# Optimization experiments

Measured on AMD Instinct MI355X. Metric: run time of the kernel, lower is better.

Reference implementation:

```python
import jax, jax.numpy as jnp
import numpy as np

EPS_MEAN = 1e-10


def setup_inputs() -> dict:
    key = jax.random.key(0)
    ks = jax.random.split(key, 16)
    B, N, F, D = 2, 512, 128, 3
    s = lambda fan_in: 1.0 / np.sqrt(fan_in)
    return {
        "h": jax.random.normal(ks[0], (B, N, F), jnp.float32),
        "coord": jax.random.normal(ks[1], (B, N, D), jnp.float32),
        "mask": jnp.ones((B, N), jnp.float32),
        "edge_w1": jax.random.normal(ks[2], (2 * F + 1, F), jnp.float32) * s(2 * F + 1),
        "edge_b1": jnp.zeros((F,), jnp.float32),
        "edge_w2": jax.random.normal(ks[3], (F, F), jnp.float32) * s(F),
        "edge_b2": jnp.zeros((F,), jnp.float32),
        "node_w1": jax.random.normal(ks[4], (2 * F, F), jnp.float32) * s(2 * F),
        "node_b1": jnp.zeros((F,), jnp.float32),
        "node_w2": jax.random.normal(ks[5], (F, F), jnp.float32) * s(F),
        "node_b2": jnp.zeros((F,), jnp.float32),
        "coord_w1": jax.random.normal(ks[6], (F, F), jnp.float32) * s(F),
        "coord_b1": jnp.zeros((F,), jnp.float32),
        # xavier_uniform with gain=0.001 -> tiny weights
        "coord_w2": jax.random.normal(ks[7], (F, 1), jnp.float32) * 0.001 * s(F),
    }


def reference(h, coord, mask, edge_w1, edge_b1, edge_w2, edge_b2,
              node_w1, node_b1, node_w2, node_b2,
              coord_w1, coord_b1, coord_w2):
    silu = jax.nn.silu
    B, N, F = h.shape
    # mask inputs
    h = h * mask[:, :, None]
    coord = coord * mask[:, :, None]
    mask2d = mask[:, :, None] * mask[:, None, :]            # [B,N,N]

    # coord2radial
    coord_diff = coord[:, :, None] - coord[:, None]          # [B,N,N,3]
    radial = jnp.sum(coord_diff ** 2, axis=-1, keepdims=True)  # [B,N,N,1]
    radial = radial * mask2d[..., None]
    coord_diff = coord_diff * mask2d[..., None]

    # edge model: source[b,i,j]=h[b,j], target[b,i,j]=h[b,i]
    source = jnp.broadcast_to(h[:, None, :, :], (B, N, N, F))
    target = jnp.broadcast_to(h[:, :, None, :], (B, N, N, F))
    edge_in = jnp.concatenate([source, target, radial], axis=-1)  # [B,N,N,2F+1]
    m = silu(edge_in @ edge_w1 + edge_b1)
    m = silu(m @ edge_w2 + edge_b2)                          # [B,N,N,F]
    m = m * mask2d[..., None]

    # coord model
    embed = silu(m @ coord_w1 + coord_b1) @ coord_w2         # [B,N,N,1]
    trans = coord_diff * embed * mask2d[..., None]           # [B,N,N,3]
    denom = jnp.sum(mask2d, axis=2, keepdims=True) + EPS_MEAN  # [B,N,1]
    coord_new = coord + jnp.sum(trans, axis=2) / denom
    coord_new = coord_new * mask[:, :, None]

    # node model
    agg = jnp.sum(m, axis=2)                                 # [B,N,F]
    node_in = jnp.concatenate([h, agg], axis=-1) * mask[:, :, None]
    out = silu(node_in @ node_w1 + node_b1) @ node_w2 + node_b2
    h_new = (h + out) * mask[:, :, None]

    return h_new, coord_new
```

## Files before the change

kernel.cpp:

```cpp
#include <hip/hip_runtime.h>

#define B_ 2
#define N_ 512
#define F_ 128
#define MSTRIDE 136

typedef __attribute__((ext_vector_type(8))) short short8;
typedef __attribute__((ext_vector_type(4))) float floatx4;

__device__ __forceinline__ float fsilu(float x) {
    float e = __expf(-x);
    return x * __builtin_amdgcn_rcpf(1.0f + e);
}
__device__ __forceinline__ unsigned pack2(float a, float b) {
    return __builtin_amdgcn_perm(__float_as_uint(b) + 0x8000u,
                                 __float_as_uint(a) + 0x8000u, 0x07060302u);
}

__global__ __launch_bounds__(256) void egcl_prep(
        const float* __restrict__ h, const float* __restrict__ mask,
        const float* __restrict__ ew1, const float* __restrict__ ew2,
        const float* __restrict__ cw1,
        float* __restrict__ Hs, float* __restrict__ Ht,
        unsigned short* __restrict__ W2P, unsigned short* __restrict__ WcP,
        float* __restrict__ msum) {
    __shared__ float hm[4 * F_];
    const int blk = blockIdx.x, tid = threadIdx.x;
    if (blk < 256) {
        const int r0 = blk * 4;
        hm[tid]       = h[r0 * F_ + tid]       * mask[r0 + (tid >> 7)];
        hm[tid + 256] = h[r0 * F_ + 256 + tid] * mask[r0 + 2 + (tid >> 7)];
        __syncthreads();
        const int col = tid & 127, half = tid >> 7;
        const float* W = ew1 + half * F_ * F_ + col;
        float a0 = 0.f, a1 = 0.f, a2 = 0.f, a3 = 0.f;
#pragma unroll 8
        for (int k = 0; k < F_; ++k) {
            float w = W[k * F_];
            a0 += hm[k] * w;
            a1 += hm[F_ + k] * w;
            a2 += hm[2 * F_ + k] * w;
            a3 += hm[3 * F_ + k] * w;
        }
        float* dst = half ? Ht : Hs;
        dst[(r0 + 0) * F_ + col] = a0;
        dst[(r0 + 1) * F_ + col] = a1;
        dst[(r0 + 2) * F_ + col] = a2;
        dst[(r0 + 3) * F_ + col] = a3;
    } else if (blk < 272) {
        const int wsel = (blk - 256) >> 3;
        const int mt = (blk - 256) & 7;
        const float* src = wsel ? cw1 : ew2;
        unsigned short* dst = wsel ? WcP : W2P;
        const int ln = tid & 63, kk = tid >> 6;
        const int qq = ln >> 4, ll = ln & 15;
#pragma unroll
        for (int rep = 0; rep < 2; ++rep) {
            const int krow = kk * 32 + qq * 8 + rep * 4;
            float f0 = src[(krow + 0) * F_ + mt * 16 + ll];
            float f1 = src[(krow + 1) * F_ + mt * 16 + ll];
            float f2 = src[(krow + 2) * F_ + mt * 16 + ll];
            float f3 = src[(krow + 3) * F_ + mt * 16 + ll];
            uint2 u = make_uint2(pack2(f0, f1), pack2(f2, f3));
            *(uint2*)(dst + ((mt * 4 + kk) * 64 + ln) * 8 + rep * 4) = u;
        }
    } else {
        const int bb = blk - 272;
        float v = mask[bb * N_ + tid] + mask[bb * N_ + 256 + tid];
        v += __shfl_xor(v, 1);  v += __shfl_xor(v, 2);
        v += __shfl_xor(v, 4);  v += __shfl_xor(v, 8);
        v += __shfl_xor(v, 16); v += __shfl_xor(v, 32);
        const int wave = tid >> 6, lane = tid & 63;
        if (lane == 0) hm[wave] = v;
        __syncthreads();
        if (tid == 0) msum[bb] = hm[0] + hm[1] + hm[2] + hm[3];
    }
}

#define L_M1   0
#define L_M    34816
#define L_HB   69632
#define L_W1R  70144
#define L_EMBP 70656
#define L_AGG  72704
#define L_HIN  73728
#define L_AGGT 74240
#define L_TL   74752
#define L_NP   75264
#define L_CSW  76288
#define L_TOTAL 76320

__global__ __launch_bounds__(512, 2) void egcl_main(
        const float* __restrict__ h, const float* __restrict__ coord,
        const float* __restrict__ mask,
        const float* __restrict__ eb1, const float* __restrict__ eb2,
        const float* __restrict__ cb1, const float* __restrict__ cw2,
        const float* __restrict__ nw1, const float* __restrict__ nb1,
        const float* __restrict__ nw2, const float* __restrict__ nb2,
        const float* __restrict__ ew1,
        const float* __restrict__ Hs, const float* __restrict__ Ht,
        const unsigned short* __restrict__ W2P,
        const unsigned short* __restrict__ WcP,
        const float* __restrict__ msum,
        float* __restrict__ out_h, float* __restrict__ out_coord) {
    extern __shared__ char smem[];
    unsigned short* m1s = (unsigned short*)(smem + L_M1);
    unsigned short* ms  = (unsigned short*)(smem + L_M);
    float* HB    = (float*)(smem + L_HB);
    float* W1R   = (float*)(smem + L_W1R);
    float* embp  = (float*)(smem + L_EMBP);
    float* aggs2 = (float*)(smem + L_AGG);
    float* hin   = (float*)(smem + L_HIN);
    float* aggt  = (float*)(smem + L_AGGT);
    float* tl    = (float*)(smem + L_TL);
    float* np    = (float*)(smem + L_NP);
    float* csw   = (float*)(smem + L_CSW);

    const int tid  = threadIdx.x;
    const int bk   = blockIdx.x;
    const int wave = tid >> 6, lane = tid & 63;
    const int q = lane >> 4, l15 = lane & 15;
    const int wg = wave & 3;
    const int g  = wave >> 2;

    short8 w2f[2][4], wcf[2][4];
#pragma unroll
    for (int s = 0; s < 2; ++s)
#pragma unroll
        for (int kk = 0; kk < 4; ++kk) {
            w2f[s][kk] = *(const short8*)(W2P + (((2 * wg + s) * 4 + kk) * 64 + lane) * 8);
            wcf[s][kk] = *(const short8*)(WcP + (((2 * wg + s) * 4 + kk) * 64 + lane) * 8);
        }
    floatx4 e2b[2], c1b[2], w2c[2];
#pragma unroll
    for (int s = 0; s < 2; ++s) {
        e2b[s] = *(const floatx4*)(eb2 + wg * 32 + s * 16 + q * 4);
        c1b[s] = *(const floatx4*)(cb1 + wg * 32 + s * 16 + q * 4);
        w2c[s] = *(const floatx4*)(cw2 + wg * 32 + s * 16 + q * 4);
    }
    const int kseg = tid & 15, jq4 = tid >> 4;

    for (int ii = 0; ii < 2; ++ii) {
        const int bi = bk + ii * 512;
        const int b  = bi >> 9;
        const float mask_i = mask[bi];
        __syncthreads();
        if (tid < F_) {
            HB[tid]  = Ht[bi * F_ + tid] + eb1[tid];
            W1R[tid] = ew1[2 * F_ * F_ + tid];
            hin[tid] = h[bi * F_ + tid] * mask_i;
        }
        const float cmi0 = coord[bi * 3 + 0] * mask_i;
        const float cmi1 = coord[bi * 3 + 1] * mask_i;
        const float cmi2 = coord[bi * 3 + 2] * mask_i;
        __syncthreads();
        float hbk[8], w1k[8];
        {
            const floatx4* hp = (const floatx4*)(HB + kseg * 8);
            const floatx4* wp = (const floatx4*)(W1R + kseg * 8);
            floatx4 a = hp[0], bb2 = hp[1], cc = wp[0], dd = wp[1];
#pragma unroll
            for (int t = 0; t < 4; ++t) {
                hbk[t] = a[t]; hbk[4 + t] = bb2[t];
                w1k[t] = cc[t]; w1k[4 + t] = dd[t];
            }
        }
        floatx4 agg0 = {0.f, 0.f, 0.f, 0.f}, agg1 = {0.f, 0.f, 0.f, 0.f};
        float cs0 = 0.f, cs1 = 0.f, cs2 = 0.f;

        for (int p = 0; p < 4; ++p) {
#pragma unroll
            for (int r = 0; r < 4; ++r) {
                int row = jq4 * 4 + r;
                int jg = b * N_ + p * 128 + row;
                float mj = mask[jg];
                float c0 = coord[jg * 3 + 0] * mj;
                float c1 = coord[jg * 3 + 1] * mj;
                float c2 = coord[jg * 3 + 2] * mj;
                float d0 = cmi0 - c0, d1 = cmi1 - c1, d2 = cmi2 - c2;
                float f2 = mask_i * mj;
                float rad = (d0 * d0 + d1 * d1 + d2 * d2) * f2;
                const floatx4* hsp = (const floatx4*)(Hs + jg * F_ + kseg * 8);
                floatx4 h0 = hsp[0], h1 = hsp[1];
                float x[8];
#pragma unroll
                for (int t = 0; t < 4; ++t) {
                    x[t]     = fsilu(h0[t] + hbk[t]     + rad * w1k[t]);
                    x[4 + t] = fsilu(h1[t] + hbk[4 + t] + rad * w1k[4 + t]);
                }
                union { short8 s8; unsigned u[4]; } pu;
                pu.u[0] = pack2(x[0], x[1]); pu.u[1] = pack2(x[2], x[3]);
                pu.u[2] = pack2(x[4], x[5]); pu.u[3] = pack2(x[6], x[7]);
                *(short8*)(m1s + row * MSTRIDE + kseg * 8) = pu.s8;
            }
            __syncthreads();
#pragma unroll
            for (int jt = 0; jt < 4; ++jt) {
                const int jrow = g * 64 + jt * 16 + l15;
                const unsigned short* m1r = m1s + jrow * MSTRIDE;
                floatx4 a0 = e2b[0], a1 = e2b[1];
#pragma unroll
                for (int kk = 0; kk < 4; ++kk) {
                    short8 bf = *(const short8*)(m1r + kk * 32 + q * 8);
                    a0 = __builtin_amdgcn_mfma_f32_16x16x32_bf16(w2f[0][kk], bf, a0, 0, 0, 0);
                    a1 = __builtin_amdgcn_mfma_f32_16x16x32_bf16(w2f[1][kk], bf, a1, 0, 0, 0);
                }
                const float f2 = mask_i * mask[b * N_ + p * 128 + jrow];
                float v0[4], v1[4];
#pragma unroll
                for (int rg = 0; rg < 4; ++rg) {
                    v0[rg] = fsilu(a0[rg]) * f2;
                    v1[rg] = fsilu(a1[rg]) * f2;
                    agg0[rg] += v0[rg];
                    agg1[rg] += v1[rg];
                }
                unsigned short* mr = ms + jrow * MSTRIDE + wg * 32 + q * 4;
                *(uint2*)(mr)      = make_uint2(pack2(v0[0], v0[1]), pack2(v0[2], v0[3]));
                *(uint2*)(mr + 16) = make_uint2(pack2(v1[0], v1[1]), pack2(v1[2], v1[3]));
            }
            __syncthreads();
#pragma unroll
            for (int jt = 0; jt < 4; ++jt) {
                const int jrow = g * 64 + jt * 16 + l15;
                const unsigned short* mr = ms + jrow * MSTRIDE;
                floatx4 a0 = c1b[0], a1 = c1b[1];
#pragma unroll
                for (int kk = 0; kk < 4; ++kk) {
                    short8 bf = *(const short8*)(mr + kk * 32 + q * 8);
                    a0 = __builtin_amdgcn_mfma_f32_16x16x32_bf16(wcf[0][kk], bf, a0, 0, 0, 0);
                    a1 = __builtin_amdgcn_mfma_f32_16x16x32_bf16(wcf[1][kk], bf, a1, 0, 0, 0);
                }
                float es = 0.f;
#pragma unroll
                for (int rg = 0; rg < 4; ++rg) {
                    es += fsilu(a0[rg]) * w2c[0][rg];
                    es += fsilu(a1[rg]) * w2c[1][rg];
                }
                es += __shfl_xor(es, 16);
                es += __shfl_xor(es, 32);
                if (q == 0) embp[wave * 64 + jt * 16 + l15] = es;
            }
            __syncthreads();
            if (tid < 128) {
                int jl = tid;
                int gg = jl >> 6, idx = jl & 63;
                float e = embp[gg * 256 + idx]       + embp[gg * 256 + 64 + idx] +
                          embp[gg * 256 + 128 + idx] + embp[gg * 256 + 192 + idx];
                int jg = b * N_ + p * 128 + jl;
                float mj = mask[jg];
                float c0 = coord[jg * 3 + 0] * mj;
                float c1 = coord[jg * 3 + 1] * mj;
                float c2 = coord[jg * 3 + 2] * mj;
                float f2 = mask_i * mj;
                float w = e * f2 * f2;
                cs0 += (cmi0 - c0) * w;
                cs1 += (cmi1 - c1) * w;
                cs2 += (cmi2 - c2) * w;
            }
        }

#pragma unroll
        for (int rg = 0; rg < 4; ++rg) {
            float v = agg0[rg];
            v += __shfl_xor(v, 1); v += __shfl_xor(v, 2);
            v += __shfl_xor(v, 4); v += __shfl_xor(v, 8);
            agg0[rg] = v;
            float u = agg1[rg];
            u += __shfl_xor(u, 1); u += __shfl_xor(u, 2);
            u += __shfl_xor(u, 4); u += __shfl_xor(u, 8);
            agg1[rg] = u;
        }
        if (l15 == 0) {
            *(floatx4*)(aggs2 + g * 128 + wg * 32 + q * 4)      = agg0;
            *(floatx4*)(aggs2 + g * 128 + wg * 32 + 16 + q * 4) = agg1;
        }
        if (wave < 2) {
            cs0 += __shfl_xor(cs0, 1); cs0 += __shfl_xor(cs0, 2);
            cs0 += __shfl_xor(cs0, 4); cs0 += __shfl_xor(cs0, 8);
            cs0 += __shfl_xor(cs0, 16); cs0 += __shfl_xor(cs0, 32);
            cs1 += __shfl_xor(cs1, 1); cs1 += __shfl_xor(cs1, 2);
            cs1 += __shfl_xor(cs1, 4); cs1 += __shfl_xor(cs1, 8);
            cs1 += __shfl_xor(cs1, 16); cs1 += __shfl_xor(cs1, 32);
            cs2 += __shfl_xor(cs2, 1); cs2 += __shfl_xor(cs2, 2);
            cs2 += __shfl_xor(cs2, 4); cs2 += __shfl_xor(cs2, 8);
            cs2 += __shfl_xor(cs2, 16); cs2 += __shfl_xor(cs2, 32);
            if (lane == 0) {
                csw[wave * 3 + 0] = cs0;
                csw[wave * 3 + 1] = cs1;
                csw[wave * 3 + 2] = cs2;
            }
        }
        __syncthreads();
        if (tid < F_) aggt[tid] = (aggs2[tid] + aggs2[128 + tid]) * mask_i;
        __syncthreads();
        if (tid < 256) {
            int half = tid >> 7, col = tid & 127;
            const float* W = nw1 + half * 128 * F_ + col;
            float s = 0.f;
            if (half == 0) {
#pragma unroll 8
                for (int k = 0; k < F_; ++k) s += hin[k] * W[k * F_];
                s *= mask_i;
            } else {
#pragma unroll 8
                for (int k = 0; k < F_; ++k) s += aggt[k] * W[k * F_];
            }
            np[tid] = s;
        }
        __syncthreads();
        if (tid < F_) tl[tid] = fsilu(np[tid] + np[128 + tid] + nb1[tid]);
        __syncthreads();
        if (tid < F_) {
            float s = nb2[tid];
#pragma unroll 8
            for (int k = 0; k < F_; ++k) s += tl[k] * nw2[k * F_ + tid];
            out_h[bi * F_ + tid] = (hin[tid] + s) * mask_i;
        } else if (tid < F_ + 3) {
            int d = tid - F_;
            float cs = csw[d] + csw[3 + d];
            float denom = mask_i * msum[b] + 1e-10f;
            float cm = (d == 0) ? cmi0 : ((d == 1) ? cmi1 : cmi2);
            out_coord[bi * 3 + d] = (cm + cs * __builtin_amdgcn_rcpf(denom)) * mask_i;
        }
    }
}

extern "C" void kernel_launch(void* const* d_in, const int* in_sizes, int n_in,
                              void* d_out, int out_size, void* d_ws, size_t ws_size,
                              hipStream_t stream) {
    const float* h     = (const float*)d_in[0];
    const float* coord = (const float*)d_in[1];
    const float* mask  = (const float*)d_in[2];
    const float* ew1   = (const float*)d_in[3];
    const float* eb1   = (const float*)d_in[4];
    const float* ew2   = (const float*)d_in[5];
    const float* eb2   = (const float*)d_in[6];
    const float* nw1   = (const float*)d_in[7];
    const float* nb1   = (const float*)d_in[8];
    const float* nw2   = (const float*)d_in[9];
    const float* nb2   = (const float*)d_in[10];
    const float* cw1   = (const float*)d_in[11];
    const float* cb1   = (const float*)d_in[12];
    const float* cw2   = (const float*)d_in[13];

    float* Hs = (float*)d_ws;
    float* Ht = Hs + B_ * N_ * F_;
    unsigned short* W2P = (unsigned short*)(Ht + B_ * N_ * F_);
    unsigned short* WcP = W2P + F_ * F_;
    float* msum = (float*)(WcP + F_ * F_);

    float* out_h = (float*)d_out;
    float* out_coord = out_h + B_ * N_ * F_;

    egcl_prep<<<274, 256, 0, stream>>>(h, mask, ew1, ew2, cw1,
                                       Hs, Ht, W2P, WcP, msum);
    egcl_main<<<512, 512, L_TOTAL, stream>>>(
        h, coord, mask, eb1, eb2, cb1, cw2, nw1, nb1, nw2, nb2, ew1,
        Hs, Ht, W2P, WcP, msum, out_h, out_coord);
}
```

Before: 215.1 us.

## Use one 256-thread block per node with 64-row j tiles in main kernel

The main kernel drops the two-wave-group, two-nodes-per-block layout. It now launches one 256-thread block per node i (1024 blocks), processing j in tiles of 64 rows with half the shared memory, and allows four blocks per CU. The prep kernel now computes 8 rows per block instead of 4, which halves its block count. This aims to improve occupancy and load balance, and to remove the cross-group aggregation. In exchange, each block runs more j-tile iterations with more barriers, and each block reloads the weight fragments.

```diff
diff --git a/kernel.cpp b/kernel.cpp
--- a/kernel.cpp
+++ b/kernel.cpp
@@ -3,6 +3,7 @@
 #define B_ 2
 #define N_ 512
 #define F_ 128
+#define TJ 64
 #define MSTRIDE 136
 
 typedef __attribute__((ext_vector_type(8))) short short8;
@@ -24,32 +25,31 @@
         float* __restrict__ Hs, float* __restrict__ Ht,
         unsigned short* __restrict__ W2P, unsigned short* __restrict__ WcP,
         float* __restrict__ msum) {
-    __shared__ float hm[4 * F_];
+    __shared__ float sh[8][F_];
     const int blk = blockIdx.x, tid = threadIdx.x;
-    if (blk < 256) {
-        const int r0 = blk * 4;
-        hm[tid]       = h[r0 * F_ + tid]       * mask[r0 + (tid >> 7)];
-        hm[tid + 256] = h[r0 * F_ + 256 + tid] * mask[r0 + 2 + (tid >> 7)];
-        __syncthreads();
+    if (blk < 128) {
+        const int r0 = blk * 8;
         const int col = tid & 127, half = tid >> 7;
+#pragma unroll
+        for (int rr = 0; rr < 4; ++rr) {
+            int row = rr * 2 + half;
+            sh[row][col] = h[(r0 + row) * F_ + col] * mask[r0 + row];
+        }
+        __syncthreads();
         const float* W = ew1 + half * F_ * F_ + col;
-        float a0 = 0.f, a1 = 0.f, a2 = 0.f, a3 = 0.f;
+        float acc[8] = {0.f, 0.f, 0.f, 0.f, 0.f, 0.f, 0.f, 0.f};
 #pragma unroll 8
         for (int k = 0; k < F_; ++k) {
             float w = W[k * F_];
-            a0 += hm[k] * w;
-            a1 += hm[F_ + k] * w;
-            a2 += hm[2 * F_ + k] * w;
-            a3 += hm[3 * F_ + k] * w;
+#pragma unroll
+            for (int r = 0; r < 8; ++r) acc[r] += sh[r][k] * w;
         }
         float* dst = half ? Ht : Hs;
-        dst[(r0 + 0) * F_ + col] = a0;
-        dst[(r0 + 1) * F_ + col] = a1;
-        dst[(r0 + 2) * F_ + col] = a2;
-        dst[(r0 + 3) * F_ + col] = a3;
-    } else if (blk < 272) {
-        const int wsel = (blk - 256) >> 3;
-        const int mt = (blk - 256) & 7;
+#pragma unroll
+        for (int r = 0; r < 8; ++r) dst[(r0 + r) * F_ + col] = acc[r];
+    } else if (blk < 144) {
+        const int wsel = (blk - 128) >> 3;
+        const int mt = (blk - 128) & 7;
         const float* src = wsel ? cw1 : ew2;
         unsigned short* dst = wsel ? WcP : W2P;
         const int ln = tid & 63, kk = tid >> 6;
@@ -65,32 +65,32 @@
             *(uint2*)(dst + ((mt * 4 + kk) * 64 + ln) * 8 + rep * 4) = u;
         }
     } else {
-        const int bb = blk - 272;
+        const int bb = blk - 144;
         float v = mask[bb * N_ + tid] + mask[bb * N_ + 256 + tid];
         v += __shfl_xor(v, 1);  v += __shfl_xor(v, 2);
         v += __shfl_xor(v, 4);  v += __shfl_xor(v, 8);
         v += __shfl_xor(v, 16); v += __shfl_xor(v, 32);
         const int wave = tid >> 6, lane = tid & 63;
-        if (lane == 0) hm[wave] = v;
-        __syncthreads();
-        if (tid == 0) msum[bb] = hm[0] + hm[1] + hm[2] + hm[3];
+        if (lane == 0) sh[0][wave] = v;
+        __syncthreads();
+        if (tid == 0) msum[bb] = sh[0][0] + sh[0][1] + sh[0][2] + sh[0][3];
     }
 }
 
 #define L_M1   0
-#define L_M    34816
-#define L_HB   69632
-#define L_W1R  70144
-#define L_EMBP 70656
-#define L_AGG  72704
-#define L_HIN  73728
-#define L_AGGT 74240
-#define L_TL   74752
-#define L_NP   75264
-#define L_CSW  76288
-#define L_TOTAL 76320
-
-__global__ __launch_bounds__(512, 2) void egcl_main(
+#define L_M    17408
+#define L_HB   34816
+#define L_W1R  35328
+#define L_EMBP 35840
+#define L_AGG  36864
+#define L_HIN  37376
+#define L_AGGT 37888
+#define L_TL   38400
+#define L_NP   38912
+#define L_CSW  39936
+#define L_TOTAL 39968
+
+__global__ __launch_bounds__(256, 4) void egcl_main(
         const float* __restrict__ h, const float* __restrict__ coord,
         const float* __restrict__ mask,
         const float* __restrict__ eb1, const float* __restrict__ eb2,
@@ -109,7 +109,7 @@
     float* HB    = (float*)(smem + L_HB);
     float* W1R   = (float*)(smem + L_W1R);
     float* embp  = (float*)(smem + L_EMBP);
-    float* aggs2 = (float*)(smem + L_AGG);
+    float* aggs  = (float*)(smem + L_AGG);
     float* hin   = (float*)(smem + L_HIN);
     float* aggt  = (float*)(smem + L_AGGT);
     float* tl    = (float*)(smem + L_TL);
@@ -117,11 +117,12 @@
     float* csw   = (float*)(smem + L_CSW);
 
     const int tid  = threadIdx.x;
-    const int bk   = blockIdx.x;
     const int wave = tid >> 6, lane = tid & 63;
     const int q = lane >> 4, l15 = lane & 15;
-    const int wg = wave & 3;
-    const int g  = wave >> 2;
+    const int wg = wave;
+    const int bi = blockIdx.x;
+    const int b  = bi >> 9;
+    const float mask_i = mask[bi];
 
     short8 w2f[2][4], wcf[2][4];
 #pragma unroll
@@ -138,190 +139,179 @@
         c1b[s] = *(const floatx4*)(cb1 + wg * 32 + s * 16 + q * 4);
         w2c[s] = *(const floatx4*)(cw2 + wg * 32 + s * 16 + q * 4);
     }
-    const int kseg = tid & 15, jq4 = tid >> 4;
-
-    for (int ii = 0; ii < 2; ++ii) {
-        const int bi = bk + ii * 512;
-        const int b  = bi >> 9;
-        const float mask_i = mask[bi];
-        __syncthreads();
-        if (tid < F_) {
-            HB[tid]  = Ht[bi * F_ + tid] + eb1[tid];
-            W1R[tid] = ew1[2 * F_ * F_ + tid];
-            hin[tid] = h[bi * F_ + tid] * mask_i;
-        }
-        const float cmi0 = coord[bi * 3 + 0] * mask_i;
-        const float cmi1 = coord[bi * 3 + 1] * mask_i;
-        const float cmi2 = coord[bi * 3 + 2] * mask_i;
-        __syncthreads();
-        float hbk[8], w1k[8];
-        {
-            const floatx4* hp = (const floatx4*)(HB + kseg * 8);
-            const floatx4* wp = (const floatx4*)(W1R + kseg * 8);
-            floatx4 a = hp[0], bb2 = hp[1], cc = wp[0], dd = wp[1];
+
+    if (tid < F_) {
+        HB[tid]  = Ht[bi * F_ + tid] + eb1[tid];
+        W1R[tid] = ew1[2 * F_ * F_ + tid];
+        hin[tid] = h[bi * F_ + tid] * mask_i;
+    }
+    const float cmi0 = coord[bi * 3 + 0] * mask_i;
+    const float cmi1 = coord[bi * 3 + 1] * mask_i;
+    const float cmi2 = coord[bi * 3 + 2] * mask_i;
+    __syncthreads();
+
+    const int kseg = tid & 15, jq = tid >> 4;
+    float hbk[8], w1k[8];
+    {
+        const floatx4* hp = (const floatx4*)(HB + kseg * 8);
+        const floatx4* wp = (const floatx4*)(W1R + kseg * 8);
+        floatx4 a = hp[0], bb2 = hp[1], cc = wp[0], dd = wp[1];
+#pragma unroll
+        for (int t = 0; t < 4; ++t) {
+            hbk[t] = a[t]; hbk[4 + t] = bb2[t];
+            w1k[t] = cc[t]; w1k[4 + t] = dd[t];
+        }
+    }
+    floatx4 agg0 = {0.f, 0.f, 0.f, 0.f}, agg1 = {0.f, 0.f, 0.f, 0.f};
+    float cs0 = 0.f, cs1 = 0.f, cs2 = 0.f;
+
+    for (int p = 0; p < N_ / TJ; ++p) {
+#pragma unroll
+        for (int r = 0; r < 4; ++r) {
+            int row = jq * 4 + r;
+            int jg = b * N_ + p * TJ + row;
+            float mj = mask[jg];
+            float c0 = coord[jg * 3 + 0] * mj;
+            float c1 = coord[jg * 3 + 1] * mj;
+            float c2 = coord[jg * 3 + 2] * mj;
+            float d0 = cmi0 - c0, d1 = cmi1 - c1, d2 = cmi2 - c2;
+            float f2 = mask_i * mj;
+            float rad = (d0 * d0 + d1 * d1 + d2 * d2) * f2;
+            const floatx4* hsp = (const floatx4*)(Hs + jg * F_ + kseg * 8);
+            floatx4 h0 = hsp[0], h1 = hsp[1];
+            float x[8];
 #pragma unroll
             for (int t = 0; t < 4; ++t) {
-                hbk[t] = a[t]; hbk[4 + t] = bb2[t];
-                w1k[t] = cc[t]; w1k[4 + t] = dd[t];
-            }
-        }
-        floatx4 agg0 = {0.f, 0.f, 0.f, 0.f}, agg1 = {0.f, 0.f, 0.f, 0.f};
-        float cs0 = 0.f, cs1 = 0.f, cs2 = 0.f;
-
-        for (int p = 0; p < 4; ++p) {
-#pragma unroll
-            for (int r = 0; r < 4; ++r) {
-                int row = jq4 * 4 + r;
-                int jg = b * N_ + p * 128 + row;
-                float mj = mask[jg];
-                float c0 = coord[jg * 3 + 0] * mj;
-                float c1 = coord[jg * 3 + 1] * mj;
-                float c2 = coord[jg * 3 + 2] * mj;
-                float d0 = cmi0 - c0, d1 = cmi1 - c1, d2 = cmi2 - c2;
-                float f2 = mask_i * mj;
-                float rad = (d0 * d0 + d1 * d1 + d2 * d2) * f2;
-                const floatx4* hsp = (const floatx4*)(Hs + jg * F_ + kseg * 8);
-                floatx4 h0 = hsp[0], h1 = hsp[1];
-                float x[8];
-#pragma unroll
-                for (int t = 0; t < 4; ++t) {
-                    x[t]     = fsilu(h0[t] + hbk[t]     + rad * w1k[t]);
-                    x[4 + t] = fsilu(h1[t] + hbk[4 + t] + rad * w1k[4 + t]);
-                }
-                union { short8 s8; unsigned u[4]; } pu;
-                pu.u[0] = pack2(x[0], x[1]); pu.u[1] = pack2(x[2], x[3]);
-                pu.u[2] = pack2(x[4], x[5]); pu.u[3] = pack2(x[6], x[7]);
-                *(short8*)(m1s + row * MSTRIDE + kseg * 8) = pu.s8;
-            }
-            __syncthreads();
-#pragma unroll
-            for (int jt = 0; jt < 4; ++jt) {
-                const int jrow = g * 64 + jt * 16 + l15;
-                const unsigned short* m1r = m1s + jrow * MSTRIDE;
-                floatx4 a0 = e2b[0], a1 = e2b[1];
-#pragma unroll
-                for (int kk = 0; kk < 4; ++kk) {
-                    short8 bf = *(const short8*)(m1r + kk * 32 + q * 8);
-                    a0 = __builtin_amdgcn_mfma_f32_16x16x32_bf16(w2f[0][kk], bf, a0, 0, 0, 0);
-                    a1 = __builtin_amdgcn_mfma_f32_16x16x32_bf16(w2f[1][kk], bf, a1, 0, 0, 0);
-                }
-                const float f2 = mask_i * mask[b * N_ + p * 128 + jrow];
-                float v0[4], v1[4];
-#pragma unroll
-                for (int rg = 0; rg < 4; ++rg) {
-                    v0[rg] = fsilu(a0[rg]) * f2;
-                    v1[rg] = fsilu(a1[rg]) * f2;
-                    agg0[rg] += v0[rg];
-                    agg1[rg] += v1[rg];
-                }
-                unsigned short* mr = ms + jrow * MSTRIDE + wg * 32 + q * 4;
-                *(uint2*)(mr)      = make_uint2(pack2(v0[0], v0[1]), pack2(v0[2], v0[3]));
-                *(uint2*)(mr + 16) = make_uint2(pack2(v1[0], v1[1]), pack2(v1[2], v1[3]));
-            }
-            __syncthreads();
-#pragma unroll
-            for (int jt = 0; jt < 4; ++jt) {
-                const int jrow = g * 64 + jt * 16 + l15;
-                const unsigned short* mr = ms + jrow * MSTRIDE;
-                floatx4 a0 = c1b[0], a1 = c1b[1];
-#pragma unroll
-                for (int kk = 0; kk < 4; ++kk) {
-                    short8 bf = *(const short8*)(mr + kk * 32 + q * 8);
-                    a0 = __builtin_amdgcn_mfma_f32_16x16x32_bf16(wcf[0][kk], bf, a0, 0, 0, 0);
-                    a1 = __builtin_amdgcn_mfma_f32_16x16x32_bf16(wcf[1][kk], bf, a1, 0, 0, 0);
-                }
-                float es = 0.f;
-#pragma unroll
-                for (int rg = 0; rg < 4; ++rg) {
-                    es += fsilu(a0[rg]) * w2c[0][rg];
-                    es += fsilu(a1[rg]) * w2c[1][rg];
-                }
-                es += __shfl_xor(es, 16);
-                es += __shfl_xor(es, 32);
-                if (q == 0) embp[wave * 64 + jt * 16 + l15] = es;
-            }
-            __syncthreads();
-            if (tid < 128) {
-                int jl = tid;
-                int gg = jl >> 6, idx = jl & 63;
-                float e = embp[gg * 256 + idx]       + embp[gg * 256 + 64 + idx] +
-                          embp[gg * 256 + 128 + idx] + embp[gg * 256 + 192 + idx];
-                int jg = b * N_ + p * 128 + jl;
-                float mj = mask[jg];
-                float c0 = coord[jg * 3 + 0] * mj;
-                float c1 = coord[jg * 3 + 1] * mj;
-                float c2 = coord[jg * 3 + 2] * mj;
-                float f2 = mask_i * mj;
-                float w = e * f2 * f2;
-                cs0 += (cmi0 - c0) * w;
-                cs1 += (cmi1 - c1) * w;
-                cs2 += (cmi2 - c2) * w;
-            }
-        }
-
-#pragma unroll
-        for (int rg = 0; rg < 4; ++rg) {
-            float v = agg0[rg];
-            v += __shfl_xor(v, 1); v += __shfl_xor(v, 2);
-            v += __shfl_xor(v, 4); v += __shfl_xor(v, 8);
-            agg0[rg] = v;
-            float u = agg1[rg];
-            u += __shfl_xor(u, 1); u += __shfl_xor(u, 2);
-            u += __shfl_xor(u, 4); u += __shfl_xor(u, 8);
-            agg1[rg] = u;
-        }
-        if (l15 == 0) {
-            *(floatx4*)(aggs2 + g * 128 + wg * 32 + q * 4)      = agg0;
-            *(floatx4*)(aggs2 + g * 128 + wg * 32 + 16 + q * 4) = agg1;
-        }
-        if (wave < 2) {
-            cs0 += __shfl_xor(cs0, 1); cs0 += __shfl_xor(cs0, 2);
-            cs0 += __shfl_xor(cs0, 4); cs0 += __shfl_xor(cs0, 8);
-            cs0 += __shfl_xor(cs0, 16); cs0 += __shfl_xor(cs0, 32);
-            cs1 += __shfl_xor(cs1, 1); cs1 += __shfl_xor(cs1, 2);
-            cs1 += __shfl_xor(cs1, 4); cs1 += __shfl_xor(cs1, 8);
-            cs1 += __shfl_xor(cs1, 16); cs1 += __shfl_xor(cs1, 32);
-            cs2 += __shfl_xor(cs2, 1); cs2 += __shfl_xor(cs2, 2);
-            cs2 += __shfl_xor(cs2, 4); cs2 += __shfl_xor(cs2, 8);
-            cs2 += __shfl_xor(cs2, 16); cs2 += __shfl_xor(cs2, 32);
-            if (lane == 0) {
-                csw[wave * 3 + 0] = cs0;
-                csw[wave * 3 + 1] = cs1;
-                csw[wave * 3 + 2] = cs2;
-            }
-        }
-        __syncthreads();
-        if (tid < F_) aggt[tid] = (aggs2[tid] + aggs2[128 + tid]) * mask_i;
-        __syncthreads();
-        if (tid < 256) {
-            int half = tid >> 7, col = tid & 127;
-            const float* W = nw1 + half * 128 * F_ + col;
-            float s = 0.f;
-            if (half == 0) {
+                x[t]     = fsilu(h0[t] + hbk[t]     + rad * w1k[t]);
+                x[4 + t] = fsilu(h1[t] + hbk[4 + t] + rad * w1k[4 + t]);
+            }
+            union { short8 s8; unsigned u[4]; } pu;
+            pu.u[0] = pack2(x[0], x[1]); pu.u[1] = pack2(x[2], x[3]);
+            pu.u[2] = pack2(x[4], x[5]); pu.u[3] = pack2(x[6], x[7]);
+            *(short8*)(m1s + row * MSTRIDE + kseg * 8) = pu.s8;
+        }
+        __syncthreads();
+#pragma unroll
+        for (int jt = 0; jt < 4; ++jt) {
+            const int jrow = jt * 16 + l15;
+            const unsigned short* m1r = m1s + jrow * MSTRIDE;
+            floatx4 a0 = e2b[0], a1 = e2b[1];
+#pragma unroll
+            for (int kk = 0; kk < 4; ++kk) {
+                short8 bf = *(const short8*)(m1r + kk * 32 + q * 8);
+                a0 = __builtin_amdgcn_mfma_f32_16x16x32_bf16(w2f[0][kk], bf, a0, 0, 0, 0);
+                a1 = __builtin_amdgcn_mfma_f32_16x16x32_bf16(w2f[1][kk], bf, a1, 0, 0, 0);
+            }
+            const float f2 = mask_i * mask[b * N_ + p * TJ + jrow];
+            float v0[4], v1[4];
+#pragma unroll
+            for (int rg = 0; rg < 4; ++rg) {
+                v0[rg] = fsilu(a0[rg]) * f2;
+                v1[rg] = fsilu(a1[rg]) * f2;
+                agg0[rg] += v0[rg];
+                agg1[rg] += v1[rg];
+            }
+            unsigned short* mr = ms + jrow * MSTRIDE + wg * 32 + q * 4;
+            *(uint2*)(mr)      = make_uint2(pack2(v0[0], v0[1]), pack2(v0[2], v0[3]));
+            *(uint2*)(mr + 16) = make_uint2(pack2(v1[0], v1[1]), pack2(v1[2], v1[3]));
+        }
+        __syncthreads();
+#pragma unroll
+        for (int jt = 0; jt < 4; ++jt) {
+            const int jrow = jt * 16 + l15;
+            const unsigned short* mr = ms + jrow * MSTRIDE;
+            floatx4 a0 = c1b[0], a1 = c1b[1];
+#pragma unroll
+            for (int kk = 0; kk < 4; ++kk) {
+                short8 bf = *(const short8*)(mr + kk * 32 + q * 8);
+                a0 = __builtin_amdgcn_mfma_f32_16x16x32_bf16(wcf[0][kk], bf, a0, 0, 0, 0);
+                a1 = __builtin_amdgcn_mfma_f32_16x16x32_bf16(wcf[1][kk], bf, a1, 0, 0, 0);
+            }
+            float es = 0.f;
+#pragma unroll
+            for (int rg = 0; rg < 4; ++rg) {
+                es += fsilu(a0[rg]) * w2c[0][rg];
+                es += fsilu(a1[rg]) * w2c[1][rg];
+            }
+            es += __shfl_xor(es, 16);
+            es += __shfl_xor(es, 32);
+            if (q == 0) embp[wg * 64 + jrow] = es;
+        }
+        __syncthreads();
+        if (tid < TJ) {
+            float e = embp[tid] + embp[64 + tid] + embp[128 + tid] + embp[192 + tid];
+            int jg = b * N_ + p * TJ + tid;
+            float mj = mask[jg];
+            float c0 = coord[jg * 3 + 0] * mj;
+            float c1 = coord[jg * 3 + 1] * mj;
+            float c2 = coord[jg * 3 + 2] * mj;
+            float f2 = mask_i * mj;
+            float w = e * f2 * f2;
+            cs0 += (cmi0 - c0) * w;
+            cs1 += (cmi1 - c1) * w;
+            cs2 += (cmi2 - c2) * w;
+        }
+    }
+
+#pragma unroll
+    for (int rg = 0; rg < 4; ++rg) {
+        float v = agg0[rg];
+        v += __shfl_xor(v, 1); v += __shfl_xor(v, 2);
+        v += __shfl_xor(v, 4); v += __shfl_xor(v, 8);
+        agg0[rg] = v;
+        float u = agg1[rg];
+        u += __shfl_xor(u, 1); u += __shfl_xor(u, 2);
+        u += __shfl_xor(u, 4); u += __shfl_xor(u, 8);
+        agg1[rg] = u;
+    }
+    if (l15 == 0) {
+        *(floatx4*)(aggs + wg * 32 + q * 4)      = agg0;
+        *(floatx4*)(aggs + wg * 32 + 16 + q * 4) = agg1;
+    }
+    if (wave == 0) {
+        cs0 += __shfl_xor(cs0, 1); cs0 += __shfl_xor(cs0, 2);
+        cs0 += __shfl_xor(cs0, 4); cs0 += __shfl_xor(cs0, 8);
+        cs0 += __shfl_xor(cs0, 16); cs0 += __shfl_xor(cs0, 32);
+        cs1 += __shfl_xor(cs1, 1); cs1 += __shfl_xor(cs1, 2);
+        cs1 += __shfl_xor(cs1, 4); cs1 += __shfl_xor(cs1, 8);
+        cs1 += __shfl_xor(cs1, 16); cs1 += __shfl_xor(cs1, 32);
+        cs2 += __shfl_xor(cs2, 1); cs2 += __shfl_xor(cs2, 2);
+        cs2 += __shfl_xor(cs2, 4); cs2 += __shfl_xor(cs2, 8);
+        cs2 += __shfl_xor(cs2, 16); cs2 += __shfl_xor(cs2, 32);
+        if (lane == 0) {
+            csw[0] = cs0; csw[1] = cs1; csw[2] = cs2;
+        }
+    }
+    __syncthreads();
+    if (tid < F_) aggt[tid] = aggs[tid] * mask_i;
+    __syncthreads();
+    {
+        int half = tid >> 7, col = tid & 127;
+        const float* W = nw1 + half * 128 * F_ + col;
+        float s = 0.f;
+        if (half == 0) {
 #pragma unroll 8
-                for (int k = 0; k < F_; ++k) s += hin[k] * W[k * F_];
-                s *= mask_i;
-            } else {
+            for (int k = 0; k < F_; ++k) s += hin[k] * W[k * F_];
+            s *= mask_i;
+        } else {
 #pragma unroll 8
-                for (int k = 0; k < F_; ++k) s += aggt[k] * W[k * F_];
-            }
-            np[tid] = s;
-        }
-        __syncthreads();
-        if (tid < F_) tl[tid] = fsilu(np[tid] + np[128 + tid] + nb1[tid]);
-        __syncthreads();
-        if (tid < F_) {
-            float s = nb2[tid];
+            for (int k = 0; k < F_; ++k) s += aggt[k] * W[k * F_];
+        }
+        np[tid] = s;
+    }
+    __syncthreads();
+    if (tid < F_) tl[tid] = fsilu(np[tid] + np[128 + tid] + nb1[tid]);
+    __syncthreads();
+    if (tid < F_) {
+        float s = nb2[tid];
 #pragma unroll 8
-            for (int k = 0; k < F_; ++k) s += tl[k] * nw2[k * F_ + tid];
-            out_h[bi * F_ + tid] = (hin[tid] + s) * mask_i;
-        } else if (tid < F_ + 3) {
-            int d = tid - F_;
-            float cs = csw[d] + csw[3 + d];
-            float denom = mask_i * msum[b] + 1e-10f;
-            float cm = (d == 0) ? cmi0 : ((d == 1) ? cmi1 : cmi2);
-            out_coord[bi * 3 + d] = (cm + cs * __builtin_amdgcn_rcpf(denom)) * mask_i;
-        }
+        for (int k = 0; k < F_; ++k) s += tl[k] * nw2[k * F_ + tid];
+        out_h[bi * F_ + tid] = (hin[tid] + s) * mask_i;
+    } else if (tid < F_ + 3) {
+        int d = tid - F_;
+        float denom = mask_i * msum[b] + 1e-10f;
+        float cm = (d == 0) ? cmi0 : ((d == 1) ? cmi1 : cmi2);
+        out_coord[bi * 3 + d] = (cm + csw[d] * __builtin_amdgcn_rcpf(denom)) * mask_i;
     }
 }
 
@@ -352,9 +342,9 @@
     float* out_h = (float*)d_out;
     float* out_coord = out_h + B_ * N_ * F_;
 
-    egcl_prep<<<274, 256, 0, stream>>>(h, mask, ew1, ew2, cw1,
+    egcl_prep<<<146, 256, 0, stream>>>(h, mask, ew1, ew2, cw1,
                                        Hs, Ht, W2P, WcP, msum);
-    egcl_main<<<512, 512, L_TOTAL, stream>>>(
+    egcl_main<<<B_ * N_, 256, L_TOTAL, stream>>>(
         h, coord, mask, eb1, eb2, cb1, cw2, nw1, nb1, nw2, nb2, ew1,
         Hs, Ht, W2P, WcP, msum, out_h, out_coord);
 }
```

Result: slower. 282.7 us (+31.4%).
